# Kernel optimization log

Measured on AMD Instinct MI355X. Metric: run time of the kernel, lower is better.

Reference implementation:

```python
import jax, jax.numpy as jnp
import numpy as np

N_HEAD, D_HEAD, D_MODEL = 8, 64, 512
MEM_LEN, QLEN, BSZ = 1024, 1024, 4
KLEN = MEM_LEN + QLEN
CONV_PAD = 3  # conv_size // 2 for conv_size = 7
LN_EPS = 1e-5


def setup_inputs() -> dict:
    key = jax.random.key(0)
    ks = jax.random.split(key, 16)
    s = 0.02
    inp = {
        "w": jax.random.normal(ks[0], (QLEN, BSZ, D_MODEL), jnp.float32),
        "r": jax.random.normal(ks[1], (KLEN, D_MODEL), jnp.float32),
        "mems": jax.random.normal(ks[2], (MEM_LEN, BSZ, D_MODEL), jnp.float32),
        "r_w_bias": jax.random.normal(ks[3], (N_HEAD, D_HEAD), jnp.float32) * s,
        "r_r_bias": jax.random.normal(ks[4], (N_HEAD, D_HEAD), jnp.float32) * s,
        "qkv_W": jax.random.normal(ks[5], (3 * N_HEAD * D_HEAD, D_MODEL), jnp.float32) * s,
        "r_W": jax.random.normal(ks[6], (N_HEAD * D_HEAD, D_MODEL), jnp.float32) * s,
        "conv_q_w": jax.random.normal(ks[7], (D_HEAD, D_HEAD, 7), jnp.float32) * 0.05,
        "conv_q_b": jnp.zeros((D_HEAD,), jnp.float32),
        "conv_k_w": jax.random.normal(ks[8], (D_HEAD, D_HEAD, 7), jnp.float32) * 0.05,
        "conv_k_b": jnp.zeros((D_HEAD,), jnp.float32),
        "conv_v_w": jax.random.normal(ks[9], (D_HEAD, D_HEAD, 7), jnp.float32) * 0.05,
        "conv_v_b": jnp.zeros((D_HEAD,), jnp.float32),
        "o_W": jax.random.normal(ks[10], (D_MODEL, N_HEAD * D_HEAD), jnp.float32) * s,
        "ln_g": jnp.ones((D_MODEL,), jnp.float32),
        "ln_b": jnp.zeros((D_MODEL,), jnp.float32),
        # causal-with-memory mask: query i may attend keys j <= i + MEM_LEN
        "attn_mask": jnp.arange(KLEN)[None, :] > (jnp.arange(QLEN)[:, None] + MEM_LEN),
    }
    return inp


def _conv1d(x, wt, b):
    # x: [N, C, L], wt: [O, I, K], same padding (pad=3)
    y = jax.lax.conv_general_dilated(x, wt, (1,), [(CONV_PAD, CONV_PAD)],
                                     dimension_numbers=("NCH", "OIH", "NCH"))
    return y + b[None, :, None]


def _head_conv(x, wt, b, length, bsz):
    # x: [len, b, H*Dh] -> per-head Conv1d over time -> [len, b, H, Dh]
    xh = x.reshape(length, bsz, N_HEAD, D_HEAD).transpose(2, 1, 3, 0)  # [H,b,Dh,len]
    xh = xh.reshape(N_HEAD * bsz, D_HEAD, length)
    xh = _conv1d(xh, wt, b)
    return xh.reshape(N_HEAD, bsz, D_HEAD, length).transpose(3, 1, 0, 2)  # [len,b,H,Dh]


def _rel_shift(x):
    # x: [qlen, rlen, b, n]
    q, rl, b, n = x.shape
    zp = jnp.zeros((q, 1, b, n), x.dtype)
    xp = jnp.concatenate([zp, x], axis=1).reshape(rl + 1, q, b, n)[1:]
    return xp.reshape(q, rl, b, n)


def _layer_norm(x, g, b):
    mu = jnp.mean(x, axis=-1, keepdims=True)
    var = jnp.mean(jnp.square(x - mu), axis=-1, keepdims=True)
    return (x - mu) * jax.lax.rsqrt(var + LN_EPS) * g + b


def reference(w, r, mems, r_w_bias, r_r_bias, qkv_W, r_W,
              conv_q_w, conv_q_b, conv_k_w, conv_k_b, conv_v_w, conv_v_b,
              o_W, ln_g, ln_b, attn_mask):
    qlen, bsz = w.shape[0], w.shape[1]
    cat = jnp.concatenate([mems, w], axis=0)           # [klen, b, d_model]
    klen = cat.shape[0]
    w_heads = cat @ qkv_W.T                            # [klen, b, 3*H*Dh]
    r_head_k = (r @ r_W.T).reshape(klen, N_HEAD, D_HEAD)
    q, k, v = jnp.split(w_heads, 3, axis=-1)
    q = q[-qlen:]
    # per-head conv augmentation of Q/K/V
    q = _head_conv(q, conv_q_w, conv_q_b, qlen, bsz)   # [qlen,b,H,Dh]
    k = _head_conv(k, conv_k_w, conv_k_b, klen, bsz)   # [klen,b,H,Dh]
    v = _head_conv(v, conv_v_w, conv_v_b, klen, bsz)
    scale = 1.0 / (D_HEAD ** 0.5)
    AC = jnp.einsum("ibnd,jbnd->ijbn", q + r_w_bias, k)
    BD = jnp.einsum("ibnd,jnd->ijbn", q + r_r_bias, r_head_k)
    BD = _rel_shift(BD)
    attn_score = (AC + BD) * scale                     # [qlen,klen,b,H]
    attn_score = jnp.where(attn_mask[:, :, None, None], -jnp.inf, attn_score)
    attn_prob = jax.nn.softmax(attn_score, axis=1)
    attn_vec = jnp.einsum("ijbn,jbnd->ibnd", attn_prob, v)
    attn_vec = attn_vec.reshape(qlen, bsz, N_HEAD * D_HEAD)
    attn_out = attn_vec @ o_W.T                        # [qlen,b,d_model]
    return _layer_norm(w + attn_out, ln_g, ln_b)
```

## Files before the change

kernel.cpp:

```cpp
#include <hip/hip_runtime.h>
#include <hip/hip_bf16.h>

typedef unsigned short u16;
typedef unsigned int   u32;
typedef u16 u16x8 __attribute__((ext_vector_type(8)));
typedef u16 u16x4 __attribute__((ext_vector_type(4)));
typedef float f32x4 __attribute__((ext_vector_type(4)));
typedef short s16x8 __attribute__((ext_vector_type(8)));
typedef u32 u32x4 __attribute__((ext_vector_type(4)));

__device__ __forceinline__ float b2f(u16 u) { return __uint_as_float(((u32)u) << 16); }
__device__ __forceinline__ u16 f2b(float f) {
  u32 u = __float_as_uint(f);
  u32 r = u + 0x7FFFu + ((u >> 16) & 1u);
  return (u16)(r >> 16);
}
__device__ __forceinline__ u32 f2b2(float lo, float hi) {
  __hip_bfloat162 h = __float22bfloat162_rn(make_float2(lo, hi));
  union { __hip_bfloat162 h; u32 u; } cv;
  cv.h = h;
  return cv.u;
}

#define MFMA_B16(A, B, C) __builtin_amdgcn_mfma_f32_16x16x32_bf16((A), (B), (C), 0, 0, 0)

__device__ __forceinline__ void gl16(const u16* g, u16* l) {
  __builtin_amdgcn_global_load_lds(
      (const __attribute__((address_space(1))) void*)g,
      (__attribute__((address_space(3))) void*)l, 16, 0, 0);
}

__global__ __launch_bounds__(256) void cvt_all(
    const float* __restrict__ mems, const float* __restrict__ w,
    const float* __restrict__ r, const float* __restrict__ qkvW,
    const float* __restrict__ rW, const float* __restrict__ oW,
    u16* __restrict__ catb, u16* __restrict__ rb, u16* __restrict__ qkvWb,
    u16* __restrict__ rWb, u16* __restrict__ oWb) {
  long g = ((long)blockIdx.x * 256 + threadIdx.x) * 8;
  const float* src;
  u16* dst;
  if (g < 4194304) {
    src = (g < 2097152) ? (mems + g) : (w + (g - 2097152));
    dst = catb + g;
  } else if (g < 5242880) {
    src = r + (g - 4194304);    dst = rb + (g - 4194304);
  } else if (g < 6029312) {
    src = qkvW + (g - 5242880); dst = qkvWb + (g - 5242880);
  } else if (g < 6291456) {
    src = rW + (g - 6029312);   dst = rWb + (g - 6029312);
  } else {
    src = oW + (g - 6291456);   dst = oWb + (g - 6291456);
  }
  f32x4 a = *(const f32x4*)src;
  f32x4 b = *(const f32x4*)(src + 4);
  u32x4 p = (u32x4){f2b2(a[0], a[1]), f2b2(a[2], a[3]),
                    f2b2(b[0], b[1]), f2b2(b[2], b[3])};
  *(u32x4*)dst = p;
}

__global__ __launch_bounds__(256) void cvt_w(
    const float* __restrict__ cqw, const float* __restrict__ ckw,
    const float* __restrict__ cvw, u16* __restrict__ cwb) {
  int idx = blockIdx.x * 256 + threadIdx.x;
  if (idx >= 86016) return;
  int wsel = idx / 28672, rem = idx % 28672;
  const float* src = (wsel == 0) ? cqw : ((wsel == 1) ? ckw : cvw);
  int s = rem / 4096, r2 = rem % 4096;
  int d = r2 / 64, eswz = r2 % 64;
  int e = (((eswz >> 3) ^ (d & 7)) << 3) + (eswz & 7);
  cwb[idx] = f2b(src[d * 448 + e * 7 + s]);
}

__global__ __launch_bounds__(256) void gemm_fused(
    const u16* __restrict__ catb, const u16* __restrict__ qkvWb,
    u16* __restrict__ Wh, const u16* __restrict__ rb,
    const u16* __restrict__ rWb, u16* __restrict__ Rk) {
  int bx = blockIdx.x, by = blockIdx.y;
  const u16 *A, *B;
  u16* C;
  int N;
  if (bx < 12) {
    if (bx < 4 && by < 32) return;
    A = catb; B = qkvWb; C = Wh; N = 1536;
  } else {
    if (by >= 16) return;
    A = rb; B = rWb; C = Rk; N = 512; bx = 0;
  }
  const int K = 512;
  __shared__ u16 A_s[128 * 32];
  __shared__ u16 B_s[128 * 32];
  int tid = threadIdx.x;
  int wave = tid >> 6, lane = tid & 63, quad = lane >> 4, l16 = lane & 15;
  int wr = wave >> 1, wc = wave & 1;

  f32x4 acc[4][4];
#pragma unroll
  for (int a = 0; a < 4; a++)
#pragma unroll
    for (int bb = 0; bb < 4; bb++) acc[a][bb] = (f32x4){0.f, 0.f, 0.f, 0.f};

  const u16* Ab = A + (size_t)by * 128 * K;
  const u16* Bb = B + (size_t)bx * 128 * K;
  int lrow = lane >> 2;
  int lkc  = (lane & 3) * 8;
  int L0 = wave * 2;

  for (int k0 = 0; k0 < K; k0 += 32) {
    __syncthreads();
#pragma unroll
    for (int m = 0; m < 2; m++) {
      int L = L0 + m;
      int row = L * 16 + lrow;
      gl16(Ab + (size_t)row * K + k0 + lkc, &A_s[L * 512 + lane * 8]);
      gl16(Bb + (size_t)row * K + k0 + lkc, &B_s[L * 512 + lane * 8]);
    }
    __syncthreads();

    s16x8 af[4], bf[4];
#pragma unroll
    for (int a = 0; a < 4; a++)
      af[a] = *(const s16x8*)&A_s[(wr * 64 + a * 16 + l16) * 32 + quad * 8];
#pragma unroll
    for (int bb = 0; bb < 4; bb++)
      bf[bb] = *(const s16x8*)&B_s[(wc * 64 + bb * 16 + l16) * 32 + quad * 8];
#pragma unroll
    for (int a = 0; a < 4; a++)
#pragma unroll
      for (int bb = 0; bb < 4; bb++)
        acc[a][bb] = MFMA_B16(af[a], bf[bb], acc[a][bb]);
  }

#pragma unroll
  for (int a = 0; a < 4; a++)
#pragma unroll
    for (int bb = 0; bb < 4; bb++) {
      int row = by * 128 + wr * 64 + a * 16 + quad * 4;
      int col = bx * 128 + wc * 64 + bb * 16 + l16;
#pragma unroll
      for (int reg = 0; reg < 4; reg++)
        C[(size_t)(row + reg) * N + col] = f2b(acc[a][bb][reg]);
    }
}

__global__ __launch_bounds__(256) void gemm_mfma(
    const u16* __restrict__ A, const u16* __restrict__ B,
    u16* __restrict__ C, int N, int K) {
  __shared__ u16 A_s[128 * 32];
  __shared__ u16 B_s[128 * 32];
  int tid = threadIdx.x;
  int bx = blockIdx.x, by = blockIdx.y;
  int wave = tid >> 6, lane = tid & 63, quad = lane >> 4, l16 = lane & 15;
  int wr = wave >> 1, wc = wave & 1;

  f32x4 acc[4][4];
#pragma unroll
  for (int a = 0; a < 4; a++)
#pragma unroll
    for (int bb = 0; bb < 4; bb++) acc[a][bb] = (f32x4){0.f, 0.f, 0.f, 0.f};

  const u16* Ab = A + (size_t)by * 128 * K;
  const u16* Bb = B + (size_t)bx * 128 * K;
  int lrow = lane >> 2;
  int lkc  = (lane & 3) * 8;
  int L0 = wave * 2;

  for (int k0 = 0; k0 < K; k0 += 32) {
    __syncthreads();
#pragma unroll
    for (int m = 0; m < 2; m++) {
      int L = L0 + m;
      int row = L * 16 + lrow;
      gl16(Ab + (size_t)row * K + k0 + lkc, &A_s[L * 512 + lane * 8]);
      gl16(Bb + (size_t)row * K + k0 + lkc, &B_s[L * 512 + lane * 8]);
    }
    __syncthreads();

    s16x8 af[4], bf[4];
#pragma unroll
    for (int a = 0; a < 4; a++)
      af[a] = *(const s16x8*)&A_s[(wr * 64 + a * 16 + l16) * 32 + quad * 8];
#pragma unroll
    for (int bb = 0; bb < 4; bb++)
      bf[bb] = *(const s16x8*)&B_s[(wc * 64 + bb * 16 + l16) * 32 + quad * 8];
#pragma unroll
    for (int a = 0; a < 4; a++)
#pragma unroll
      for (int bb = 0; bb < 4; bb++)
        acc[a][bb] = MFMA_B16(af[a], bf[bb], acc[a][bb]);
  }

#pragma unroll
  for (int a = 0; a < 4; a++)
#pragma unroll
    for (int bb = 0; bb < 4; bb++) {
      int row = by * 128 + wr * 64 + a * 16 + quad * 4;
      int col = bx * 128 + wc * 64 + bb * 16 + l16;
#pragma unroll
      for (int reg = 0; reg < 4; reg++)
        C[(size_t)(row + reg) * N + col] = f2b(acc[a][bb][reg]);
    }
}

__global__ __launch_bounds__(256) void conv_fused(
    const u16* __restrict__ Wh, const u16* __restrict__ cwb,
    const float* __restrict__ cqb, const float* __restrict__ ckb,
    const float* __restrict__ cvb,
    u16* __restrict__ qpost, u16* __restrict__ kpost, u16* __restrict__ vpostT) {
  __shared__ u16 wT_s[7 * 4096];
  __shared__ u16 in_s[134 * 64];
  int tile = blockIdx.x;
  int part, t0, len, tshift, vt;
  const float* cbp;
  const u16* cwp;
  u16* outp;
  if (tile < 8) {
    part = 0; t0 = tile * 128; len = 1024; tshift = 1024; vt = 0;
    cbp = cqb; cwp = cwb; outp = qpost;
  } else if (tile < 24) {
    part = 1; t0 = (tile - 8) * 128; len = 2048; tshift = 0; vt = 0;
    cbp = ckb; cwp = cwb + 28672; outp = kpost;
  } else {
    part = 2; t0 = (tile - 24) * 128; len = 2048; tshift = 0; vt = 1;
    cbp = cvb; cwp = cwb + 57344; outp = vpostT;
  }
  int tid = threadIdx.x;
  int b = blockIdx.y, n = blockIdx.z;
  int wave = tid >> 6, lane = tid & 63, quad = lane >> 4, l16 = lane & 15;

  for (int idx = tid * 8; idx < 28672; idx += 2048)
    *(u16x8*)&wT_s[idx] = *(const u16x8*)(cwp + idx);
  {
    int e8 = tid & 7;
    int colb = part * 512 + n * 64 + e8 * 8;
    for (int r = tid >> 3; r < 134; r += 32) {
      int tt = t0 + r - 3;
      u16x8 v = {0, 0, 0, 0, 0, 0, 0, 0};
      if (tt >= 0 && tt < len)
        v = *(const u16x8*)(Wh + (size_t)((tt + tshift) * 4 + b) * 1536 + colb);
      *(u16x8*)&in_s[r * 64 + ((e8 ^ (r & 7)) << 3)] = v;
    }
  }
  __syncthreads();

  f32x4 acc[2][4];
#pragma unroll
  for (int mt = 0; mt < 2; mt++)
#pragma unroll
    for (int nn = 0; nn < 4; nn++) acc[mt][nn] = (f32x4){0.f, 0.f, 0.f, 0.f};

#pragma unroll
  for (int s = 0; s < 7; s++) {
#pragma unroll
    for (int ks = 0; ks < 2; ks++) {
      int eb = ks * 4 + quad;
      s16x8 af[2];
#pragma unroll
      for (int mt = 0; mt < 2; mt++) {
        int r = wave * 32 + mt * 16 + l16 + s;
        af[mt] = *(const s16x8*)&in_s[r * 64 + ((eb ^ (r & 7)) << 3)];
      }
#pragma unroll
      for (int nn = 0; nn < 4; nn++) {
        int d = nn * 16 + l16;
        s16x8 bf = *(const s16x8*)&wT_s[s * 4096 + d * 64 + ((eb ^ (d & 7)) << 3)];
        acc[0][nn] = MFMA_B16(af[0], bf, acc[0][nn]);
        acc[1][nn] = MFMA_B16(af[1], bf, acc[1][nn]);
      }
    }
  }

  float bias[4];
#pragma unroll
  for (int nn = 0; nn < 4; nn++) bias[nn] = cbp[nn * 16 + l16];

  if (!vt) {
#pragma unroll
    for (int mt = 0; mt < 2; mt++)
#pragma unroll
      for (int nn = 0; nn < 4; nn++) {
        int col = nn * 16 + l16;
#pragma unroll
        for (int reg = 0; reg < 4; reg++) {
          int t = t0 + wave * 32 + mt * 16 + quad * 4 + reg;
          outp[(size_t)((t * 4 + b) * 8 + n) * 64 + col] = f2b(acc[mt][nn][reg] + bias[nn]);
        }
      }
  } else {
    __syncthreads();
    u16* T = wT_s;
#pragma unroll
    for (int mt = 0; mt < 2; mt++)
#pragma unroll
      for (int nn = 0; nn < 4; nn++) {
        union { u32 u[2]; u16x4 v; } pk;
        pk.u[0] = f2b2(acc[mt][nn][0] + bias[nn], acc[mt][nn][1] + bias[nn]);
        pk.u[1] = f2b2(acc[mt][nn][2] + bias[nn], acc[mt][nn][3] + bias[nn]);
        *(u16x4*)&T[(nn * 16 + l16) * 136 + wave * 32 + mt * 16 + quad * 4] = pk.v;
      }
    __syncthreads();
    int dS = tid >> 2, tq = tid & 3;
    u16* gdst = outp + ((size_t)(b * 8 + n) * 64 + dS) * 2048 + t0 + tq * 32;
    const u16* tsrc = &T[dS * 136 + tq * 32];
#pragma unroll
    for (int c = 0; c < 4; c++)
      *(u16x8*)(gdst + c * 8) = *(const u16x8*)(tsrc + c * 8);
  }
}

__global__ __launch_bounds__(256) void attn_mfma(
    const u16* __restrict__ qpost, const u16* __restrict__ kpost,
    const u16* __restrict__ vpostT, const u16* __restrict__ Rk,
    const float* __restrict__ rwb, const float* __restrict__ rrb,
    u16* __restrict__ av_out) {
  __shared__ u16 K_s[64 * 64];
  __shared__ u16 V_s[64 * 64];
  __shared__ u16 R_s[128 * 64];
  __shared__ u16 BD_s[4][80 * 20];
  __shared__ u16 P_s[4][16 * 64];
  int tid = threadIdx.x;
  int bxr = blockIdx.x;
  int it = (bxr & 1) ? (15 - (bxr >> 1)) : (bxr >> 1);
  int i0 = it * 64, b = blockIdx.y, n = blockIdx.z;
  int wave = tid >> 6, lane = tid & 63, quad = lane >> 4, l16 = lane & 15;
  int i0w = i0 + wave * 16;
  int rbaseW = 48 - wave * 16;
  int rbase = 960 - i0;
  int ntiles = it + 17;
  const float SC = 0.125f * 1.44269504f;

  s16x8 aw[2], ar[2];
  {
    int ig = i0w + l16;
    const u16* qp = qpost + ((size_t)((ig * 4 + b) * 8 + n)) * 64;
#pragma unroll
    for (int ks = 0; ks < 2; ks++) {
      int d0 = ks * 32 + quad * 8;
      u16x8 qv = *(const u16x8*)(qp + d0);
      union { u32x4 u; s16x8 s; } pw, pr;
#pragma unroll
      for (int e2 = 0; e2 < 4; e2++) {
        float qa = b2f(qv[2 * e2]), qb = b2f(qv[2 * e2 + 1]);
        pw.u[e2] = f2b2(qa + rwb[n * 64 + d0 + 2 * e2], qb + rwb[n * 64 + d0 + 2 * e2 + 1]);
        pr.u[e2] = f2b2(qa + rrb[n * 64 + d0 + 2 * e2], qb + rrb[n * 64 + d0 + 2 * e2 + 1]);
      }
      aw[ks] = pw.s;
      ar[ks] = pr.s;
    }
  }

  {
    int rrI = tid >> 1, h = tid & 1;
    int g = rbase + rrI;
    int prow = g & 127;
    const u16* rp2 = Rk + (size_t)g * 512 + n * 64 + h * 32;
#pragma unroll
    for (int c = 0; c < 4; c++) {
      int kb = h * 4 + c;
      *(u16x8*)&R_s[prow * 64 + ((kb ^ (prow & 7)) << 3)] = *(const u16x8*)(rp2 + c * 8);
    }
  }

  f32x4 O[4];
#pragma unroll
  for (int c = 0; c < 4; c++) O[c] = (f32x4){0.f, 0.f, 0.f, 0.f};
  float l4[4] = {0.f, 0.f, 0.f, 0.f};

  int jl = tid >> 2, q4 = tid & 3;
  u16x8 kv0, kv1, vv0, vv1, rv0, rv1;
  {
    size_t src = ((size_t)(jl * 4 + b) * 8 + n) * 64 + q4 * 16;
    kv0 = *(const u16x8*)(kpost + src);
    kv1 = *(const u16x8*)(kpost + src + 8);
    const u16* vsrc = vpostT + ((size_t)(b * 8 + n) * 64 + jl) * 2048 + q4 * 16;
    vv0 = *(const u16x8*)(vsrc);
    vv1 = *(const u16x8*)(vsrc + 8);
  }
  {
    int g = rbase + 128 + jl;
    rv0 = (u16x8){0, 0, 0, 0, 0, 0, 0, 0};
    rv1 = rv0;
    if (g < 2048) {
      const u16* rp2 = Rk + (size_t)g * 512 + n * 64 + q4 * 16;
      rv0 = *(const u16x8*)(rp2);
      rv1 = *(const u16x8*)(rp2 + 8);
    }
  }

  for (int t = 0; t < ntiles; t++) {
    int j0 = t * 64;
    __syncthreads();
    *(u16x8*)&K_s[jl * 64 + (((2 * q4) ^ (jl & 7)) << 3)] = kv0;
    *(u16x8*)&K_s[jl * 64 + (((2 * q4 + 1) ^ (jl & 7)) << 3)] = kv1;
    *(u16x8*)&V_s[jl * 64 + (((2 * q4) ^ (jl & 7)) << 3)] = vv0;
    *(u16x8*)&V_s[jl * 64 + (((2 * q4 + 1) ^ (jl & 7)) << 3)] = vv1;
    if (t > 0) {
      int g = rbase + j0 + 64 + jl;
      int prow = g & 127;
      *(u16x8*)&R_s[prow * 64 + (((2 * q4) ^ (prow & 7)) << 3)] = rv0;
      *(u16x8*)&R_s[prow * 64 + (((2 * q4 + 1) ^ (prow & 7)) << 3)] = rv1;
    }
    __syncthreads();

    if (t + 1 < ntiles) {
      int j0n = j0 + 64;
      size_t src = ((size_t)((j0n + jl) * 4 + b) * 8 + n) * 64 + q4 * 16;
      kv0 = *(const u16x8*)(kpost + src);
      kv1 = *(const u16x8*)(kpost + src + 8);
      const u16* vsrc = vpostT + ((size_t)(b * 8 + n) * 64 + jl) * 2048 + j0n + q4 * 16;
      vv0 = *(const u16x8*)(vsrc);
      vv1 = *(const u16x8*)(vsrc + 8);
      int g = rbase + j0n + 64 + jl;
      rv0 = (u16x8){0, 0, 0, 0, 0, 0, 0, 0};
      rv1 = rv0;
      if (g < 2048) {
        const u16* rp2 = Rk + (size_t)g * 512 + n * 64 + q4 * 16;
        rv0 = *(const u16x8*)(rp2);
        rv1 = *(const u16x8*)(rp2 + 8);
      }
    }

    f32x4 sc4[4];
#pragma unroll
    for (int c = 0; c < 4; c++) {
      f32x4 tt = (f32x4){0.f, 0.f, 0.f, 0.f};
#pragma unroll
      for (int ks = 0; ks < 2; ks++) {
        int j = c * 16 + l16;
        int kb = ks * 4 + quad;
        s16x8 kf = *(const s16x8*)&K_s[j * 64 + ((kb ^ (j & 7)) << 3)];
        tt = MFMA_B16(aw[ks], kf, tt);
      }
      sc4[c] = tt;
    }
    int rbj = rbase + j0 + rbaseW;
#pragma unroll
    for (int cb = 0; cb < 5; cb++) {
      f32x4 tt = (f32x4){0.f, 0.f, 0.f, 0.f};
#pragma unroll
      for (int ks = 0; ks < 2; ks++) {
        int prow = (rbj + cb * 16 + l16) & 127;
        int kb = ks * 4 + quad;
        s16x8 rf = *(const s16x8*)&R_s[prow * 64 + ((kb ^ (prow & 7)) << 3)];
        tt = MFMA_B16(ar[ks], rf, tt);
      }
      union { u32 u[2]; u16x4 v; } pk;
      pk.u[0] = f2b2(tt[0], tt[1]);
      pk.u[1] = f2b2(tt[2], tt[3]);
      *(u16x4*)&BD_s[wave][(cb * 16 + l16) * 20 + quad * 4] = pk.v;
    }

#pragma unroll
    for (int c = 0; c < 4; c++)
#pragma unroll
      for (int reg = 0; reg < 4; reg++) {
        int iw = quad * 4 + reg;
        int uw = c * 16 + l16 + 15 - iw;
        float bd = b2f(BD_s[wave][uw * 20 + iw]);
        float val = (sc4[c][reg] + bd) * SC;
        int jg = j0 + c * 16 + l16;
        float p = (jg > i0w + iw + 1024) ? 0.f : __builtin_amdgcn_exp2f(val);
        l4[reg] += p;
        int jb = c * 2 + (l16 >> 3);
        P_s[wave][iw * 64 + ((jb ^ (iw & 7)) << 3) + (l16 & 7)] = f2b(p);
      }

#pragma unroll
    for (int cd = 0; cd < 4; cd++) {
      int d = cd * 16 + l16;
#pragma unroll
      for (int ks = 0; ks < 2; ks++) {
        int kb = ks * 4 + quad;
        s16x8 pf = *(const s16x8*)&P_s[wave][l16 * 64 + ((kb ^ (l16 & 7)) << 3)];
        s16x8 vf = *(const s16x8*)&V_s[d * 64 + ((kb ^ (d & 7)) << 3)];
        O[cd] = MFMA_B16(pf, vf, O[cd]);
      }
    }
  }

#pragma unroll
  for (int off = 1; off < 16; off <<= 1)
#pragma unroll
    for (int reg = 0; reg < 4; reg++) l4[reg] += __shfl_xor(l4[reg], off);

#pragma unroll
  for (int reg = 0; reg < 4; reg++) {
    float inv = 1.0f / l4[reg];
    int ig2 = i0w + quad * 4 + reg;
#pragma unroll
    for (int cd = 0; cd < 4; cd++)
      av_out[((size_t)(ig2 * 4 + b)) * 512 + n * 64 + cd * 16 + l16] =
          f2b(O[cd][reg] * inv);
  }
}

__global__ __launch_bounds__(64) void lnorm(
    const float* __restrict__ w, const u16* __restrict__ ao,
    const float* __restrict__ g, const float* __restrict__ bb,
    float* __restrict__ out) {
  int row = blockIdx.x, t = threadIdx.x;
  const float* wp = w + (size_t)row * 512 + t * 8;
  const u16* ap = ao + (size_t)row * 512 + t * 8;
  f32x4 w0 = *(const f32x4*)wp;
  f32x4 w1 = *(const f32x4*)(wp + 4);
  u16x8 av = *(const u16x8*)ap;
  float x[8];
  float sum = 0.f;
#pragma unroll
  for (int e = 0; e < 4; e++) {
    x[e] = w0[e] + b2f(av[e]);
    x[4 + e] = w1[e] + b2f(av[4 + e]);
  }
#pragma unroll
  for (int e = 0; e < 8; e++) sum += x[e];
#pragma unroll
  for (int off = 1; off < 64; off <<= 1) sum += __shfl_xor(sum, off);
  float mu = sum * (1.0f / 512.0f);
  float vs = 0.f;
#pragma unroll
  for (int e = 0; e < 8; e++) {
    float d = x[e] - mu;
    vs += d * d;
  }
#pragma unroll
  for (int off = 1; off < 64; off <<= 1) vs += __shfl_xor(vs, off);
  float rs = rsqrtf(vs * (1.0f / 512.0f) + 1e-5f);
  f32x4 g0 = *(const f32x4*)(g + t * 8);
  f32x4 g1 = *(const f32x4*)(g + t * 8 + 4);
  f32x4 b0 = *(const f32x4*)(bb + t * 8);
  f32x4 b1 = *(const f32x4*)(bb + t * 8 + 4);
  f32x4 o0, o1;
#pragma unroll
  for (int e = 0; e < 4; e++) {
    o0[e] = (x[e] - mu) * rs * g0[e] + b0[e];
    o1[e] = (x[4 + e] - mu) * rs * g1[e] + b1[e];
  }
  float* op = out + (size_t)row * 512 + t * 8;
  *(f32x4*)op = o0;
  *(f32x4*)(op + 4) = o1;
}

extern "C" void kernel_launch(void* const* d_in, const int* in_sizes, int n_in,
                              void* d_out, int out_size, void* d_ws, size_t ws_size,
                              hipStream_t stream) {
  (void)in_sizes; (void)n_in; (void)out_size;
  const float* w    = (const float*)d_in[0];
  const float* r    = (const float*)d_in[1];
  const float* mems = (const float*)d_in[2];
  const float* rwb  = (const float*)d_in[3];
  const float* rrb  = (const float*)d_in[4];
  const float* qkvW = (const float*)d_in[5];
  const float* rW   = (const float*)d_in[6];
  const float* cqw  = (const float*)d_in[7];
  const float* cqb  = (const float*)d_in[8];
  const float* ckw  = (const float*)d_in[9];
  const float* ckb  = (const float*)d_in[10];
  const float* cvw  = (const float*)d_in[11];
  const float* cvb  = (const float*)d_in[12];
  const float* oW   = (const float*)d_in[13];
  const float* lng  = (const float*)d_in[14];
  const float* lnb  = (const float*)d_in[15];

  u16* ws     = (u16*)d_ws;
  u16* Wh     = ws;
  u16* qpost  = Wh + 12582912;
  u16* kpost  = qpost + 2097152;
  u16* vpostT = kpost + 4194304;
  u16* Rk     = vpostT + 4194304;
  u16* av     = Rk + 1048576;
  u16* aout   = av + 2097152;
  u16* qkvWb  = aout + 2097152;
  u16* rWb    = qkvWb + 786432;
  u16* oWb    = rWb + 262144;
  u16* cwb    = oWb + 262144;
  u16* catb   = av;
  u16* rb     = qpost;
  if (ws_size < 59416576ull) return;

  cvt_all<<<3200, 256, 0, stream>>>(mems, w, r, qkvW, rW, oW, catb, rb, qkvWb, rWb, oWb);
  cvt_w<<<336, 256, 0, stream>>>(cqw, ckw, cvw, cwb);
  gemm_fused<<<dim3(13, 64), 256, 0, stream>>>(catb, qkvWb, Wh, rb, rWb, Rk);
  conv_fused<<<dim3(40, 4, 8), 256, 0, stream>>>(Wh, cwb, cqb, ckb, cvb, qpost, kpost, vpostT);
  attn_mfma<<<dim3(16, 4, 8), 256, 0, stream>>>(qpost, kpost, vpostT, Rk, rwb, rrb, av);
  gemm_mfma<<<dim3(4, 32), 256, 0, stream>>>(av, oWb, aout, 512, 512);
  lnorm<<<4096, 64, 0, stream>>>(w, aout, lng, lnb, (float*)d_out);
}
```

Before: 239.3 us.

## Double-buffer attention K/V/R register prefetch, set MFMA priority, merge conv-weight cast

The attention kernel now prefetches K, V and R tiles two iterations ahead using A/B register sets instead of one, to hide more global-load latency behind compute. It raises wave priority around the MFMA sections, and reads the BD values into registers before the softmax loop. Separately, the conv-weight conversion kernel is folded into cvt_all as extra blocks, removing one launch. The change increases register pressure, which may reduce occupancy.

```diff
diff --git a/kernel.cpp b/kernel.cpp
--- a/kernel.cpp
+++ b/kernel.cpp
@@ -34,8 +34,21 @@
     const float* __restrict__ mems, const float* __restrict__ w,
     const float* __restrict__ r, const float* __restrict__ qkvW,
     const float* __restrict__ rW, const float* __restrict__ oW,
+    const float* __restrict__ cqw, const float* __restrict__ ckw,
+    const float* __restrict__ cvw,
     u16* __restrict__ catb, u16* __restrict__ rb, u16* __restrict__ qkvWb,
-    u16* __restrict__ rWb, u16* __restrict__ oWb) {
+    u16* __restrict__ rWb, u16* __restrict__ oWb, u16* __restrict__ cwb) {
+  if (blockIdx.x >= 3200) {
+    int idx = (blockIdx.x - 3200) * 256 + threadIdx.x;
+    if (idx >= 86016) return;
+    int wsel = idx / 28672, rem = idx % 28672;
+    const float* src = (wsel == 0) ? cqw : ((wsel == 1) ? ckw : cvw);
+    int s = rem / 4096, r2 = rem % 4096;
+    int d = r2 / 64, eswz = r2 % 64;
+    int e = (((eswz >> 3) ^ (d & 7)) << 3) + (eswz & 7);
+    cwb[idx] = f2b(src[d * 448 + e * 7 + s]);
+    return;
+  }
   long g = ((long)blockIdx.x * 256 + threadIdx.x) * 8;
   const float* src;
   u16* dst;
@@ -56,19 +69,6 @@
   u32x4 p = (u32x4){f2b2(a[0], a[1]), f2b2(a[2], a[3]),
                     f2b2(b[0], b[1]), f2b2(b[2], b[3])};
   *(u32x4*)dst = p;
-}
-
-__global__ __launch_bounds__(256) void cvt_w(
-    const float* __restrict__ cqw, const float* __restrict__ ckw,
-    const float* __restrict__ cvw, u16* __restrict__ cwb) {
-  int idx = blockIdx.x * 256 + threadIdx.x;
-  if (idx >= 86016) return;
-  int wsel = idx / 28672, rem = idx % 28672;
-  const float* src = (wsel == 0) ? cqw : ((wsel == 1) ? ckw : cvw);
-  int s = rem / 4096, r2 = rem % 4096;
-  int d = r2 / 64, eswz = r2 % 64;
-  int e = (((eswz >> 3) ^ (d & 7)) << 3) + (eswz & 7);
-  cwb[idx] = f2b(src[d * 448 + e * 7 + s]);
 }
 
 __global__ __launch_bounds__(256) void gemm_fused(
@@ -307,6 +307,45 @@
   }
 }
 
+#define LOADKV(K0, K1, V0, V1, J0N)                                         \
+  do {                                                                      \
+    size_t src_ = ((size_t)(((J0N) + jl) * 4 + b) * 8 + n) * 64 + q4 * 16;  \
+    K0 = *(const u16x8*)(kpost + src_);                                     \
+    K1 = *(const u16x8*)(kpost + src_ + 8);                                 \
+    const u16* vs_ = vpostT + ((size_t)(b * 8 + n) * 64 + jl) * 2048 +      \
+                     (J0N) + q4 * 16;                                       \
+    V0 = *(const u16x8*)(vs_);                                              \
+    V1 = *(const u16x8*)(vs_ + 8);                                          \
+  } while (0)
+
+#define LOADR(R0, R1, G)                                                    \
+  do {                                                                      \
+    int g_ = (G) + jl;                                                      \
+    R0 = (u16x8){0, 0, 0, 0, 0, 0, 0, 0};                                   \
+    R1 = R0;                                                                \
+    if (g_ < 2048) {                                                        \
+      const u16* rp_ = Rk + (size_t)g_ * 512 + n * 64 + q4 * 16;            \
+      R0 = *(const u16x8*)(rp_);                                            \
+      R1 = *(const u16x8*)(rp_ + 8);                                        \
+    }                                                                       \
+  } while (0)
+
+#define STAGEKV(K0, K1, V0, V1)                                             \
+  do {                                                                      \
+    *(u16x8*)&K_s[jl * 64 + (((2 * q4) ^ (jl & 7)) << 3)] = K0;             \
+    *(u16x8*)&K_s[jl * 64 + (((2 * q4 + 1) ^ (jl & 7)) << 3)] = K1;         \
+    *(u16x8*)&V_s[jl * 64 + (((2 * q4) ^ (jl & 7)) << 3)] = V0;             \
+    *(u16x8*)&V_s[jl * 64 + (((2 * q4 + 1) ^ (jl & 7)) << 3)] = V1;         \
+  } while (0)
+
+#define STAGER(R0, R1, G)                                                   \
+  do {                                                                      \
+    int g_ = (G) + jl;                                                      \
+    int prow_ = g_ & 127;                                                   \
+    *(u16x8*)&R_s[prow_ * 64 + (((2 * q4) ^ (prow_ & 7)) << 3)] = R0;       \
+    *(u16x8*)&R_s[prow_ * 64 + (((2 * q4 + 1) ^ (prow_ & 7)) << 3)] = R1;   \
+  } while (0)
+
 __global__ __launch_bounds__(256) void attn_mfma(
     const u16* __restrict__ qpost, const u16* __restrict__ kpost,
     const u16* __restrict__ vpostT, const u16* __restrict__ Rk,
@@ -366,59 +405,38 @@
   float l4[4] = {0.f, 0.f, 0.f, 0.f};
 
   int jl = tid >> 2, q4 = tid & 3;
-  u16x8 kv0, kv1, vv0, vv1, rv0, rv1;
-  {
-    size_t src = ((size_t)(jl * 4 + b) * 8 + n) * 64 + q4 * 16;
-    kv0 = *(const u16x8*)(kpost + src);
-    kv1 = *(const u16x8*)(kpost + src + 8);
-    const u16* vsrc = vpostT + ((size_t)(b * 8 + n) * 64 + jl) * 2048 + q4 * 16;
-    vv0 = *(const u16x8*)(vsrc);
-    vv1 = *(const u16x8*)(vsrc + 8);
-  }
-  {
-    int g = rbase + 128 + jl;
-    rv0 = (u16x8){0, 0, 0, 0, 0, 0, 0, 0};
-    rv1 = rv0;
-    if (g < 2048) {
-      const u16* rp2 = Rk + (size_t)g * 512 + n * 64 + q4 * 16;
-      rv0 = *(const u16x8*)(rp2);
-      rv1 = *(const u16x8*)(rp2 + 8);
-    }
-  }
+  u16x8 kvA0, kvA1, vvA0, vvA1, rvA0, rvA1;
+  u16x8 kvB0, kvB1, vvB0, vvB1, rvB0, rvB1;
+  LOADKV(kvA0, kvA1, vvA0, vvA1, 0);
+  rvA0 = (u16x8){0, 0, 0, 0, 0, 0, 0, 0};
+  rvA1 = rvA0;
+  LOADKV(kvB0, kvB1, vvB0, vvB1, 64);
+  LOADR(rvB0, rvB1, rbase + 128);
 
   for (int t = 0; t < ntiles; t++) {
     int j0 = t * 64;
     __syncthreads();
-    *(u16x8*)&K_s[jl * 64 + (((2 * q4) ^ (jl & 7)) << 3)] = kv0;
-    *(u16x8*)&K_s[jl * 64 + (((2 * q4 + 1) ^ (jl & 7)) << 3)] = kv1;
-    *(u16x8*)&V_s[jl * 64 + (((2 * q4) ^ (jl & 7)) << 3)] = vv0;
-    *(u16x8*)&V_s[jl * 64 + (((2 * q4 + 1) ^ (jl & 7)) << 3)] = vv1;
-    if (t > 0) {
-      int g = rbase + j0 + 64 + jl;
-      int prow = g & 127;
-      *(u16x8*)&R_s[prow * 64 + (((2 * q4) ^ (prow & 7)) << 3)] = rv0;
-      *(u16x8*)&R_s[prow * 64 + (((2 * q4 + 1) ^ (prow & 7)) << 3)] = rv1;
-    }
-    __syncthreads();
-
-    if (t + 1 < ntiles) {
-      int j0n = j0 + 64;
-      size_t src = ((size_t)((j0n + jl) * 4 + b) * 8 + n) * 64 + q4 * 16;
-      kv0 = *(const u16x8*)(kpost + src);
-      kv1 = *(const u16x8*)(kpost + src + 8);
-      const u16* vsrc = vpostT + ((size_t)(b * 8 + n) * 64 + jl) * 2048 + j0n + q4 * 16;
-      vv0 = *(const u16x8*)(vsrc);
-      vv1 = *(const u16x8*)(vsrc + 8);
-      int g = rbase + j0n + 64 + jl;
-      rv0 = (u16x8){0, 0, 0, 0, 0, 0, 0, 0};
-      rv1 = rv0;
-      if (g < 2048) {
-        const u16* rp2 = Rk + (size_t)g * 512 + n * 64 + q4 * 16;
-        rv0 = *(const u16x8*)(rp2);
-        rv1 = *(const u16x8*)(rp2 + 8);
-      }
-    }
-
+    if (!(t & 1)) {
+      STAGEKV(kvA0, kvA1, vvA0, vvA1);
+      if (t > 0) STAGER(rvA0, rvA1, rbase + j0 + 64);
+    } else {
+      STAGEKV(kvB0, kvB1, vvB0, vvB1);
+      STAGER(rvB0, rvB1, rbase + j0 + 64);
+    }
+    __syncthreads();
+
+    int tp = t + 2;
+    if (tp < ntiles) {
+      if (!(t & 1)) {
+        LOADKV(kvA0, kvA1, vvA0, vvA1, tp * 64);
+        LOADR(rvA0, rvA1, rbase + tp * 64 + 64);
+      } else {
+        LOADKV(kvB0, kvB1, vvB0, vvB1, tp * 64);
+        LOADR(rvB0, rvB1, rbase + tp * 64 + 64);
+      }
+    }
+
+    __builtin_amdgcn_s_setprio(1);
     f32x4 sc4[4];
 #pragma unroll
     for (int c = 0; c < 4; c++) {
@@ -448,15 +466,24 @@
       pk.u[1] = f2b2(tt[2], tt[3]);
       *(u16x4*)&BD_s[wave][(cb * 16 + l16) * 20 + quad * 4] = pk.v;
     }
-
+    __builtin_amdgcn_s_setprio(0);
+
+    float bdv[4][4];
+#pragma unroll
+    for (int reg = 0; reg < 4; reg++) {
+      int iw = quad * 4 + reg;
+#pragma unroll
+      for (int c = 0; c < 4; c++) {
+        int uw = c * 16 + l16 + 15 - iw;
+        bdv[c][reg] = b2f(BD_s[wave][uw * 20 + iw]);
+      }
+    }
 #pragma unroll
     for (int c = 0; c < 4; c++)
 #pragma unroll
       for (int reg = 0; reg < 4; reg++) {
         int iw = quad * 4 + reg;
-        int uw = c * 16 + l16 + 15 - iw;
-        float bd = b2f(BD_s[wave][uw * 20 + iw]);
-        float val = (sc4[c][reg] + bd) * SC;
+        float val = (sc4[c][reg] + bdv[c][reg]) * SC;
         int jg = j0 + c * 16 + l16;
         float p = (jg > i0w + iw + 1024) ? 0.f : __builtin_amdgcn_exp2f(val);
         l4[reg] += p;
@@ -464,6 +491,7 @@
         P_s[wave][iw * 64 + ((jb ^ (iw & 7)) << 3) + (l16 & 7)] = f2b(p);
       }
 
+    __builtin_amdgcn_s_setprio(1);
 #pragma unroll
     for (int cd = 0; cd < 4; cd++) {
       int d = cd * 16 + l16;
@@ -475,6 +503,7 @@
         O[cd] = MFMA_B16(pf, vf, O[cd]);
       }
     }
+    __builtin_amdgcn_s_setprio(0);
   }
 
 #pragma unroll
@@ -576,8 +605,8 @@
   u16* rb     = qpost;
   if (ws_size < 59416576ull) return;
 
-  cvt_all<<<3200, 256, 0, stream>>>(mems, w, r, qkvW, rW, oW, catb, rb, qkvWb, rWb, oWb);
-  cvt_w<<<336, 256, 0, stream>>>(cqw, ckw, cvw, cwb);
+  cvt_all<<<3536, 256, 0, stream>>>(mems, w, r, qkvW, rW, oW, cqw, ckw, cvw,
+                                    catb, rb, qkvWb, rWb, oWb, cwb);
   gemm_fused<<<dim3(13, 64), 256, 0, stream>>>(catb, qkvWb, Wh, rb, rWb, Rk);
   conv_fused<<<dim3(40, 4, 8), 256, 0, stream>>>(Wh, cwb, cqb, ckb, cvb, qpost, kpost, vpostT);
   attn_mfma<<<dim3(16, 4, 8), 256, 0, stream>>>(qpost, kpost, vpostT, Rk, rwb, rrb, av);
```

Result: no change. 242.6 us (+1.4%).
